# Performance work log

Hardware: AMD Instinct MI355X
Metric: run time of the kernel (lower is better)

The kernel has to match this reference:

```python
import jax, jax.numpy as jnp
import numpy as np

DIM = 256
K = 255
PAD = K // 2  # 127, 'same' padding


def _dwconv(x, w, b, pad_h, pad_w):
    # x: [N, C, H, W]; w: [C, 1, kh, kw] (OIHW with feature_group_count=C)
    y = jax.lax.conv_general_dilated(
        x, w,
        window_strides=(1, 1),
        padding=((pad_h, pad_h), (pad_w, pad_w)),
        dimension_numbers=("NCHW", "OIHW", "NCHW"),
        feature_group_count=x.shape[1],
    )
    return y + b[None, :, None, None]


def setup_inputs() -> dict:
    key = jax.random.key(0)
    k1, k2, k3, k4, k5 = jax.random.split(key, 5)
    x = jax.random.normal(k1, (10, DIM, 128, 128), dtype=jnp.float32)
    # depthwise weights, scaled like torch's kaiming-uniform fan_in=K
    scale = 1.0 / np.sqrt(K)
    wh = jax.random.uniform(k2, (DIM, 1, K, 1), jnp.float32, -scale, scale)
    bh = jax.random.uniform(k3, (DIM,), jnp.float32, -scale, scale)
    ww = jax.random.uniform(k4, (DIM, 1, 1, K), jnp.float32, -scale, scale)
    bw = jax.random.uniform(k5, (DIM,), jnp.float32, -scale, scale)
    return {"x": x, "wh": wh, "bh": bh, "ww": ww, "bw": bw}


def reference(x, wh, bh, ww, bw):
    # conv_h: (K,1) depthwise conv, padding (K//2, 0)
    x = _dwconv(x, wh, bh, PAD, 0)
    # conv_w: (1,K) depthwise conv, padding (0, K//2)
    x = _dwconv(x, ww, bw, 0, PAD)
    return x
```

## Files before the change

kernel.cpp:

```cpp
#include <hip/hip_runtime.h>

#define HW 128
#define KTAPS 255
#define DIMC 256

typedef short short8 __attribute__((ext_vector_type(8)));
typedef float f32x16 __attribute__((ext_vector_type(16)));

__device__ __forceinline__ short f2bf(float f) {
    return __builtin_bit_cast(short, (__bf16)f);
}
__device__ __forceinline__ int pad16(int c) { return c + (c >> 3); }


__global__ __launch_bounds__(256, 2)
void sep_conv255_mfma(const float* __restrict__ x,
                      const float* __restrict__ wh,
                      const float* __restrict__ bh,
                      const float* __restrict__ ww,
                      const float* __restrict__ bw,
                      float* __restrict__ out) {
    __shared__ __align__(16) short P1[2304 * 8];
    __shared__ __align__(16) short P2[2304 * 8];

    const int blk  = blockIdx.x;
    const int c    = blk & (DIMC - 1);
    const int tid  = threadIdx.x;
    const int lane = tid & 63;
    const int wv   = tid >> 6;

    const float* __restrict__ xc  = x + (size_t)blk * (HW * HW);
    float* __restrict__ zc        = out + (size_t)blk * (HW * HW);
    const float* __restrict__ whc = wh + c * KTAPS;
    const float* __restrict__ wwc = ww + c * KTAPS;

#pragma unroll
    for (int i = 0; i < 8; ++i) {
        const int ch = tid + (i << 8);
        const int lc = ch & 63;
        const int ks = (ch >> 6) & 7;
        const int tm = ch >> 9;
        const int m  = (tm << 5) + (lc & 31);
        const int kb = (ks << 4) + ((lc >> 5) << 3);
        const float* wp = whc + (127 + kb - m);
        short8 v;
#pragma unroll
        for (int j = 0; j < 8; ++j) v[j] = f2bf(wp[j]);
        *reinterpret_cast<short8*>(&P2[pad16(ch) * 8]) = v;
    }
    {
        const int n  = tid & 127;
        const int bc = (n >> 5) << 3;
#pragma unroll 2
        for (int i = 0; i < 8; ++i) {
            const int rg = (tid >> 7) + (i << 1);
            const int r0 = rg << 3;
            float xv[8];
#pragma unroll
            for (int j = 0; j < 8; ++j) xv[j] = xc[(r0 + j) * HW + n];
            short8 v;
#pragma unroll
            for (int j = 0; j < 8; ++j) v[j] = f2bf(xv[j]);
            const int ch = (bc + (r0 >> 4)) * 64 + (n & 31) + (((r0 >> 3) & 1) << 5);
            *reinterpret_cast<short8*>(&P1[pad16(ch) * 8]) = v;
        }
    }
    __syncthreads();

    f32x16 acc[4];
#pragma unroll
    for (int t = 0; t < 4; ++t)
#pragma unroll
        for (int j = 0; j < 16; ++j) acc[t][j] = 0.0f;

#pragma unroll
    for (int ks = 0; ks < 8; ++ks) {
        const short8 a = *reinterpret_cast<const short8*>(
            &P2[pad16(((wv << 3) + ks) * 64 + lane) * 8]);
#pragma unroll
        for (int t = 0; t < 4; ++t) {
            const short8 b = *reinterpret_cast<const short8*>(
                &P1[pad16(((t << 3) + ks) * 64 + lane) * 8]);
            acc[t] = __builtin_amdgcn_mfma_f32_32x32x16_bf16(a, b, acc[t], 0, 0, 0);
        }
    }
    __syncthreads();

    const float bhv = bh[c];
    {
        const int hbase = (wv << 5) + ((lane >> 5) << 2);
        const int s31   = lane & 31;
#pragma unroll
        for (int t = 0; t < 4; ++t) {
            const int s  = (t << 5) + s31;
            const int cb = ((wv << 3) + (s >> 4)) * 64 + (((s >> 3) & 1) << 5);
            const int jj = s & 7;
#pragma unroll
            for (int r = 0; r < 16; ++r) {
                const int h = hbase + (r & 3) + ((r >> 2) << 3);
                P1[pad16(cb + (h & 31)) * 8 + jj] = f2bf(acc[t][r] + bhv);
            }
        }
    }
#pragma unroll
    for (int i = 0; i < 8; ++i) {
        const int ch = tid + (i << 8);
        const int lc = ch & 63;
        const int ks = (ch >> 6) & 7;
        const int tn = ch >> 9;
        const int n  = (tn << 5) + (lc & 31);
        const int kb = (ks << 4) + ((lc >> 5) << 3);
        const float* wp = wwc + (127 + kb - n);
        short8 v;
#pragma unroll
        for (int j = 0; j < 8; ++j) v[j] = f2bf(wp[j]);
        *reinterpret_cast<short8*>(&P2[pad16(ch) * 8]) = v;
    }
    __syncthreads();

#pragma unroll
    for (int t = 0; t < 4; ++t)
#pragma unroll
        for (int j = 0; j < 16; ++j) acc[t][j] = 0.0f;

#pragma unroll
    for (int ks = 0; ks < 8; ++ks) {
        const short8 a = *reinterpret_cast<const short8*>(
            &P1[pad16(((wv << 3) + ks) * 64 + lane) * 8]);
#pragma unroll
        for (int t = 0; t < 4; ++t) {
            const short8 b = *reinterpret_cast<const short8*>(
                &P2[pad16(((t << 3) + ks) * 64 + lane) * 8]);
            acc[t] = __builtin_amdgcn_mfma_f32_32x32x16_bf16(a, b, acc[t], 0, 0, 0);
        }
    }

    const float bwv = bw[c];
    {
        const int hbase = (wv << 5) + ((lane >> 5) << 2);
        const int w31   = lane & 31;
#pragma unroll
        for (int t = 0; t < 4; ++t) {
            const int w2 = (t << 5) + w31;
#pragma unroll
            for (int r = 0; r < 16; ++r) {
                const int h = hbase + (r & 3) + ((r >> 2) << 3);
                zc[h * HW + w2] = acc[t][r] + bwv;
            }
        }
    }
}

extern "C" void kernel_launch(void* const* d_in, const int* in_sizes, int n_in,
                              void* d_out, int out_size, void* d_ws, size_t ws_size,
                              hipStream_t stream) {
    const float* x  = (const float*)d_in[0];
    const float* wh = (const float*)d_in[1];
    const float* bh = (const float*)d_in[2];
    const float* ww = (const float*)d_in[3];
    const float* bw = (const float*)d_in[4];
    float* outp = (float*)d_out;

    const int nbatch = in_sizes[0] / (DIMC * HW * HW);
    dim3 grid(nbatch * DIMC);
    dim3 block(256);
    hipLaunchKernelGGL(sep_conv255_mfma, grid, block, 0, stream,
                       x, wh, bh, ww, bw, outp);
}
```

Before: 296.6 us.

## Prebuild bf16 Toeplitz weight fragments and keep intermediate in registers

A new pre-kernel builds the banded Toeplitz weight fragments for both convolutions in bf16, once per channel, into the workspace. The main kernel loads them straight into registers instead of rebuilding them in LDS for every (batch, channel) block. The first GEMM is reorganized (transposed operand roles) so its accumulator output is reused directly as the A operand of the second GEMM. This drops the LDS round trip, one buffer and two barriers, and raises the occupancy target to 3 blocks. The cost is an extra launch, global fragment reads per block and higher register pressure.

```diff
diff --git a/kernel.cpp b/kernel.cpp
--- a/kernel.cpp
+++ b/kernel.cpp
@@ -6,22 +6,52 @@
 
 typedef short short8 __attribute__((ext_vector_type(8)));
 typedef float f32x16 __attribute__((ext_vector_type(16)));
+typedef unsigned int uint4v __attribute__((ext_vector_type(4)));
 
 __device__ __forceinline__ short f2bf(float f) {
     return __builtin_bit_cast(short, (__bf16)f);
 }
+__device__ __forceinline__ unsigned int pkbf(float a, float b) {
+    unsigned int lo = (unsigned short)__builtin_bit_cast(unsigned short, (__bf16)a);
+    unsigned int hi = (unsigned short)__builtin_bit_cast(unsigned short, (__bf16)b);
+    return lo | (hi << 16);
+}
 __device__ __forceinline__ int pad16(int c) { return c + (c >> 3); }
 
+__global__ void build_wfrags(const float* __restrict__ wh,
+                             const float* __restrict__ ww,
+                             short8* __restrict__ wf) {
+    const int c   = blockIdx.x;
+    const int tid = threadIdx.x;
+    const float* __restrict__ whc = wh + c * KTAPS;
+    const float* __restrict__ wwc = ww + c * KTAPS;
+    short8* __restrict__ w1 = wf + (size_t)c * 2048;
+    short8* __restrict__ w2 = wf + (size_t)(DIMC + c) * 2048;
+#pragma unroll
+    for (int i = 0; i < 8; ++i) {
+        const int ch = tid + (i << 8);
+        const int ln = ch & 63;
+        const int ks = (ch >> 6) & 7;
+        const int nb = ch >> 9;
+        const int n  = (nb << 5) + (ln & 31);
+        const int kb = (ks << 4) + ((ln >> 5) << 3);
+        const float* p1 = whc + (127 + kb - n);
+        const float* p2 = wwc + (127 + kb - n);
+        short8 v1, v2;
+#pragma unroll
+        for (int j = 0; j < 8; ++j) { v1[j] = f2bf(p1[j]); v2[j] = f2bf(p2[j]); }
+        w1[ch] = v1;
+        w2[ch] = v2;
+    }
+}
 
-__global__ __launch_bounds__(256, 2)
-void sep_conv255_mfma(const float* __restrict__ x,
-                      const float* __restrict__ wh,
-                      const float* __restrict__ bh,
-                      const float* __restrict__ ww,
-                      const float* __restrict__ bw,
-                      float* __restrict__ out) {
-    __shared__ __align__(16) short P1[2304 * 8];
-    __shared__ __align__(16) short P2[2304 * 8];
+__global__ __launch_bounds__(256, 3)
+void sep_conv255_mfma2(const float* __restrict__ x,
+                       const float* __restrict__ bh,
+                       const float* __restrict__ bw,
+                       const short8* __restrict__ wf,
+                       float* __restrict__ out) {
+    __shared__ __align__(16) short8 XF[2304];
 
     const int blk  = blockIdx.x;
     const int c    = blk & (DIMC - 1);
@@ -29,124 +59,86 @@
     const int lane = tid & 63;
     const int wv   = tid >> 6;
 
-    const float* __restrict__ xc  = x + (size_t)blk * (HW * HW);
-    float* __restrict__ zc        = out + (size_t)blk * (HW * HW);
-    const float* __restrict__ whc = wh + c * KTAPS;
-    const float* __restrict__ wwc = ww + c * KTAPS;
+    const float* __restrict__ xc = x + (size_t)blk * (HW * HW);
+    float* __restrict__ zc       = out + (size_t)blk * (HW * HW);
+    const short8* __restrict__ w1 = wf + (size_t)c * 2048;
+    const short8* __restrict__ w2 = wf + (size_t)(DIMC + c) * 2048;
 
+    {
+        const int s    = tid & 127;
+        const int mp   = (s & ~12) | ((s & 4) << 1) | ((s & 8) >> 1);
+        const int half = tid >> 7;
 #pragma unroll
-    for (int i = 0; i < 8; ++i) {
-        const int ch = tid + (i << 8);
-        const int lc = ch & 63;
-        const int ks = (ch >> 6) & 7;
-        const int tm = ch >> 9;
-        const int m  = (tm << 5) + (lc & 31);
-        const int kb = (ks << 4) + ((lc >> 5) << 3);
-        const float* wp = whc + (127 + kb - m);
-        short8 v;
-#pragma unroll
-        for (int j = 0; j < 8; ++j) v[j] = f2bf(wp[j]);
-        *reinterpret_cast<short8*>(&P2[pad16(ch) * 8]) = v;
-    }
-    {
-        const int n  = tid & 127;
-        const int bc = (n >> 5) << 3;
-#pragma unroll 2
         for (int i = 0; i < 8; ++i) {
-            const int rg = (tid >> 7) + (i << 1);
+            const int rg = half + (i << 1);
             const int r0 = rg << 3;
             float xv[8];
 #pragma unroll
-            for (int j = 0; j < 8; ++j) xv[j] = xc[(r0 + j) * HW + n];
-            short8 v;
+            for (int j = 0; j < 8; ++j) xv[j] = xc[(r0 + j) * HW + s];
+            uint4v d;
 #pragma unroll
-            for (int j = 0; j < 8; ++j) v[j] = f2bf(xv[j]);
-            const int ch = (bc + (r0 >> 4)) * 64 + (n & 31) + (((r0 >> 3) & 1) << 5);
-            *reinterpret_cast<short8*>(&P1[pad16(ch) * 8]) = v;
+            for (int q = 0; q < 4; ++q) d[q] = pkbf(xv[2 * q], xv[2 * q + 1]);
+            const int chunk = ((mp >> 5) * 8 + (rg >> 1)) * 64 + (mp & 31) + ((rg & 1) << 5);
+            XF[pad16(chunk)] = __builtin_bit_cast(short8, d);
         }
     }
+
+    short8 b1[8];
+#pragma unroll
+    for (int ks = 0; ks < 8; ++ks) b1[ks] = w1[((wv << 3) + ks) * 64 + lane];
+    const float bhv = bh[c];
+    const float bwv = bw[c];
+
     __syncthreads();
 
-    f32x16 acc[4];
+    f32x16 acc1[4];
 #pragma unroll
     for (int t = 0; t < 4; ++t)
 #pragma unroll
-        for (int j = 0; j < 16; ++j) acc[t][j] = 0.0f;
+        for (int j = 0; j < 16; ++j) acc1[t][j] = 0.0f;
 
 #pragma unroll
     for (int ks = 0; ks < 8; ++ks) {
-        const short8 a = *reinterpret_cast<const short8*>(
-            &P2[pad16(((wv << 3) + ks) * 64 + lane) * 8]);
 #pragma unroll
-        for (int t = 0; t < 4; ++t) {
-            const short8 b = *reinterpret_cast<const short8*>(
-                &P1[pad16(((t << 3) + ks) * 64 + lane) * 8]);
-            acc[t] = __builtin_amdgcn_mfma_f32_32x32x16_bf16(a, b, acc[t], 0, 0, 0);
-        }
-    }
-    __syncthreads();
-
-    const float bhv = bh[c];
-    {
-        const int hbase = (wv << 5) + ((lane >> 5) << 2);
-        const int s31   = lane & 31;
-#pragma unroll
-        for (int t = 0; t < 4; ++t) {
-            const int s  = (t << 5) + s31;
-            const int cb = ((wv << 3) + (s >> 4)) * 64 + (((s >> 3) & 1) << 5);
-            const int jj = s & 7;
-#pragma unroll
-            for (int r = 0; r < 16; ++r) {
-                const int h = hbase + (r & 3) + ((r >> 2) << 3);
-                P1[pad16(cb + (h & 31)) * 8 + jj] = f2bf(acc[t][r] + bhv);
-            }
-        }
-    }
-#pragma unroll
-    for (int i = 0; i < 8; ++i) {
-        const int ch = tid + (i << 8);
-        const int lc = ch & 63;
-        const int ks = (ch >> 6) & 7;
-        const int tn = ch >> 9;
-        const int n  = (tn << 5) + (lc & 31);
-        const int kb = (ks << 4) + ((lc >> 5) << 3);
-        const float* wp = wwc + (127 + kb - n);
-        short8 v;
-#pragma unroll
-        for (int j = 0; j < 8; ++j) v[j] = f2bf(wp[j]);
-        *reinterpret_cast<short8*>(&P2[pad16(ch) * 8]) = v;
-    }
-    __syncthreads();
-
-#pragma unroll
-    for (int t = 0; t < 4; ++t)
-#pragma unroll
-        for (int j = 0; j < 16; ++j) acc[t][j] = 0.0f;
-
-#pragma unroll
-    for (int ks = 0; ks < 8; ++ks) {
-        const short8 a = *reinterpret_cast<const short8*>(
-            &P1[pad16(((wv << 3) + ks) * 64 + lane) * 8]);
-#pragma unroll
-        for (int t = 0; t < 4; ++t) {
-            const short8 b = *reinterpret_cast<const short8*>(
-                &P2[pad16(((t << 3) + ks) * 64 + lane) * 8]);
-            acc[t] = __builtin_amdgcn_mfma_f32_32x32x16_bf16(a, b, acc[t], 0, 0, 0);
+        for (int mb = 0; mb < 4; ++mb) {
+            const short8 a = XF[pad16(((mb << 3) + ks) * 64 + lane)];
+            acc1[mb] = __builtin_amdgcn_mfma_f32_32x32x16_bf16(a, b1[ks], acc1[mb], 0, 0, 0);
         }
     }
 
-    const float bwv = bw[c];
-    {
-        const int hbase = (wv << 5) + ((lane >> 5) << 2);
-        const int w31   = lane & 31;
+    short8 a2[8];
 #pragma unroll
-        for (int t = 0; t < 4; ++t) {
-            const int w2 = (t << 5) + w31;
+    for (int mb = 0; mb < 4; ++mb) {
+        unsigned int d[8];
 #pragma unroll
-            for (int r = 0; r < 16; ++r) {
-                const int h = hbase + (r & 3) + ((r >> 2) << 3);
-                zc[h * HW + w2] = acc[t][r] + bwv;
-            }
+        for (int i = 0; i < 8; ++i)
+            d[i] = pkbf(acc1[mb][2 * i] + bhv, acc1[mb][2 * i + 1] + bhv);
+        uint4v lo, hi;
+#pragma unroll
+        for (int q = 0; q < 4; ++q) { lo[q] = d[q]; hi[q] = d[4 + q]; }
+        a2[2 * mb]     = __builtin_bit_cast(short8, lo);
+        a2[2 * mb + 1] = __builtin_bit_cast(short8, hi);
+    }
+
+    const int hb = (wv << 5) + ((lane >> 5) << 2);
+    const int wl = lane & 31;
+#pragma unroll
+    for (int t = 0; t < 4; ++t) {
+        short8 b2[8];
+#pragma unroll
+        for (int ks = 0; ks < 8; ++ks) b2[ks] = w2[((t << 3) + ks) * 64 + lane];
+        f32x16 acc2;
+#pragma unroll
+        for (int j = 0; j < 16; ++j) acc2[j] = 0.0f;
+#pragma unroll
+        for (int ks = 0; ks < 8; ++ks)
+            acc2 = __builtin_amdgcn_mfma_f32_32x32x16_bf16(a2[ks], b2[ks], acc2, 0, 0, 0);
+
+        float* __restrict__ zp = zc + (t << 5) + wl;
+#pragma unroll
+        for (int r = 0; r < 16; ++r) {
+            const int h = hb + (r & 3) + ((r >> 2) << 3);
+            zp[h * HW] = acc2[r] + bwv;
         }
     }
 }
@@ -160,10 +152,11 @@
     const float* ww = (const float*)d_in[3];
     const float* bw = (const float*)d_in[4];
     float* outp = (float*)d_out;
+    short8* wf = (short8*)d_ws;
 
     const int nbatch = in_sizes[0] / (DIMC * HW * HW);
-    dim3 grid(nbatch * DIMC);
-    dim3 block(256);
-    hipLaunchKernelGGL(sep_conv255_mfma, grid, block, 0, stream,
-                       x, wh, bh, ww, bw, outp);
+
+    hipLaunchKernelGGL(build_wfrags, dim3(DIMC), dim3(256), 0, stream, wh, ww, wf);
+    hipLaunchKernelGGL(sep_conv255_mfma2, dim3(nbatch * DIMC), dim3(256), 0, stream,
+                       x, bh, bw, wf, outp);
 }
```

Result: no change. 301.4 us (+1.6%).
